# Performance work log

Measured on AMD Instinct MI355X. Metric: run time of the kernel, lower is better.

The kernel has to match this reference:

```python
import jax, jax.numpy as jnp
import numpy as np

M, D, G, E = 100000, 64, 1024, 1600000  # nodes, hidden, graphs, edges


def setup_inputs() -> dict:
    key = jax.random.key(0)
    k1, k2, k3, k4 = jax.random.split(key, 4)
    x = jax.random.normal(k1, (M, D), dtype=jnp.float32)
    batch = jnp.sort(jax.random.randint(k2, (M,), 0, G)).astype(jnp.int64)
    edge = jax.random.randint(k3, (2, E), 0, M).astype(jnp.int64)
    # nn.Linear(D, 1) parameters
    att_w = jax.random.normal(k4, (1, D), dtype=jnp.float32) * (1.0 / np.sqrt(D))
    att_b = jnp.zeros((1,), dtype=jnp.float32)
    return {"x": x, "att_w": att_w, "att_b": att_b, "batch": batch, "edge": edge}


def reference(x, att_w, att_b, batch, edge):
    # imp = attention(x): [M, 1] -> [M]
    imp = (x @ att_w.T + att_b)[:, 0]
    # scatter_softmax of imp over graph segments (batch)
    seg_max = jax.ops.segment_max(imp, batch, num_segments=G)
    e = jnp.exp(imp - seg_max[batch])
    denom = jax.ops.segment_sum(e, batch, num_segments=G)
    a = e / denom[batch]  # [M]
    # (degree branch is dead code when degree=False; degree softmax unused)
    # per-node weighted outer product imp_k * x_k x_k^T, scatter-summed per graph
    wj = (a[:, None] * x)[:, :, None] * x[:, None, :]  # [M, D, D]
    out = jax.ops.segment_sum(wj, batch, num_segments=G)  # [G, D, D]
    # Triuvec: upper-triangular (incl. diagonal) vectorization, row-major
    iu = jnp.triu_indices(D)
    return out[:, iu[0], iu[1]]  # [G, D*(D+1)/2]
```

## Files before the change

kernel.cpp:

```cpp
#include <hip/hip_runtime.h>
#include <math.h>


#define DDIM 64
#define NTRI 2080
#define CAP  2048
#define TILE 8

__device__ __forceinline__ float dot_row_w(const float* __restrict__ row,
                                           const float* __restrict__ sW) {
    float d = 0.f;
#pragma unroll
    for (int k = 0; k < 16; ++k) {
        const float4 v = ((const float4*)row)[k];
        const float4 w = ((const float4*)sW)[k];
        d = fmaf(v.x, w.x, d);
        d = fmaf(v.y, w.y, d);
        d = fmaf(v.z, w.z, d);
        d = fmaf(v.w, w.w, d);
    }
    return d;
}

__global__ void __launch_bounds__(256)
attention_sop_kernel(const float* __restrict__ x,
                     const float* __restrict__ att_w,
                     const float* __restrict__ att_b,
                     const int*   __restrict__ batch,
                     float*       __restrict__ out,
                     int M)
{
    const int g   = blockIdx.x;
    const int tid = threadIdx.x;

    __shared__ float sW[DDIM];
    __shared__ float sB;
    __shared__ float sImp[CAP];
    __shared__ float sRed[8];
    __shared__ float sXr[TILE * DDIM];
    __shared__ float sYs[TILE * DDIM];
    __shared__ int   sBounds[2];

    if (tid == 0) {
        int lo = 0, hi = M;
        while (lo < hi) { int mid = (lo + hi) >> 1; if (batch[mid] < g) lo = mid + 1; else hi = mid; }
        sBounds[0] = lo;
        int lo2 = lo, hi2 = M;
        while (lo2 < hi2) { int mid = (lo2 + hi2) >> 1; if (batch[mid] < g + 1) lo2 = mid + 1; else hi2 = mid; }
        sBounds[1] = lo2;
    }
    if (tid < DDIM) sW[tid] = att_w[tid];
    if (tid == DDIM) sB = att_b[0];
    __syncthreads();

    const int s = sBounds[0];
    const int e = sBounds[1];
    const int n = e - s;
    const float bb = sB;

    float* og = out + (size_t)g * NTRI;

    if (n == 0) {
        for (int idx = tid; idx < NTRI; idx += 256) og[idx] = 0.f;
        return;
    }

    float lmax = -INFINITY;
    for (int idx = tid; idx < n; idx += 256) {
        const float* row = x + (size_t)(s + idx) * DDIM;
        float d = dot_row_w(row, sW) + bb;
        if (idx < CAP) sImp[idx] = d;
        lmax = fmaxf(lmax, d);
    }
#pragma unroll
    for (int off = 32; off > 0; off >>= 1)
        lmax = fmaxf(lmax, __shfl_down(lmax, off, 64));
    const int wid = tid >> 6, lane = tid & 63;
    if (lane == 0) sRed[wid] = lmax;
    __syncthreads();
    if (tid == 0) {
        float mx = fmaxf(fmaxf(sRed[0], sRed[1]), fmaxf(sRed[2], sRed[3]));
        sRed[4] = mx;
    }
    __syncthreads();
    const float mx = sRed[4];

    float lsum = 0.f;
    for (int idx = tid; idx < n; idx += 256) {
        float d;
        if (idx < CAP) d = sImp[idx];
        else           d = dot_row_w(x + (size_t)(s + idx) * DDIM, sW) + bb;
        float ev = __expf(d - mx);
        if (idx < CAP) sImp[idx] = ev;
        lsum += ev;
    }
#pragma unroll
    for (int off = 32; off > 0; off >>= 1)
        lsum += __shfl_down(lsum, off, 64);
    if (lane == 0) sRed[wid] = lsum;
    __syncthreads();
    if (tid == 0) {
        float denom = sRed[0] + sRed[1] + sRed[2] + sRed[3];
        sRed[5] = 1.0f / denom;
    }
    __syncthreads();
    const float inv = sRed[5];

    const int ty = tid >> 4, tx = tid & 15;
    const int i0 = ty * 4, j0 = tx * 4;
    float acc[4][4];
#pragma unroll
    for (int a = 0; a < 4; ++a)
#pragma unroll
        for (int b = 0; b < 4; ++b) acc[a][b] = 0.f;

    for (int t0 = 0; t0 < n; t0 += TILE) {
        const int nt = min(TILE, n - t0);
        __syncthreads();
        for (int idx = tid; idx < nt * DDIM; idx += 256) {
            const int nn   = idx >> 6;
            const int gidx = t0 + nn;
            float c;
            if (gidx < CAP) {
                c = sImp[gidx] * inv;
            } else {
                float d  = dot_row_w(x + (size_t)(s + gidx) * DDIM, sW) + bb;
                c = __expf(d - mx) * inv;
            }
            const float v = x[(size_t)(s + t0) * DDIM + idx];
            sXr[idx] = v;
            sYs[idx] = v * c;
        }
        __syncthreads();
        for (int nn = 0; nn < nt; ++nn) {
            const float4 yi = *(const float4*)&sYs[nn * DDIM + i0];
            const float4 xj = *(const float4*)&sXr[nn * DDIM + j0];
            const float yv[4] = {yi.x, yi.y, yi.z, yi.w};
            const float xv[4] = {xj.x, xj.y, xj.z, xj.w};
#pragma unroll
            for (int a = 0; a < 4; ++a)
#pragma unroll
                for (int b = 0; b < 4; ++b)
                    acc[a][b] = fmaf(yv[a], xv[b], acc[a][b]);
        }
    }

#pragma unroll
    for (int a = 0; a < 4; ++a) {
        const int i = i0 + a;
        const int base = i * DDIM - (i * (i - 1)) / 2;
#pragma unroll
        for (int b = 0; b < 4; ++b) {
            const int j = j0 + b;
            if (j >= i) og[base + (j - i)] = acc[a][b];
        }
    }
}

extern "C" void kernel_launch(void* const* d_in, const int* in_sizes, int n_in,
                              void* d_out, int out_size, void* d_ws, size_t ws_size,
                              hipStream_t stream) {
    const float* x     = (const float*)d_in[0];
    const float* att_w = (const float*)d_in[1];
    const float* att_b = (const float*)d_in[2];
    const int*   batch = (const int*)d_in[3];
    float* out = (float*)d_out;

    const int M = in_sizes[0] / DDIM;
    const int G = out_size / NTRI;

    attention_sop_kernel<<<G, 256, 0, stream>>>(x, att_w, att_b, batch, out, M);
}
```

Baseline: 111.6 us.

## Split attention scores into a prep kernel and double-buffer node tiles in SOP kernel

Moves the per-node attention dot product and segment-boundary discovery into a separate fully parallel prep kernel that writes scores and segment starts to workspace. This replaces the per-block serial binary search and the repeated row dot products. The outer-product kernel now uses larger tiles of 32 nodes with register-prefetched double buffering, and applies the softmax weight on the fly instead of keeping a scaled copy. In exchange it adds a second launch and workspace traffic, and it relies on the workspace being large enough.

```diff
diff --git a/kernel.cpp b/kernel.cpp
--- a/kernel.cpp
+++ b/kernel.cpp
@@ -4,105 +4,96 @@
 
 #define DDIM 64
 #define NTRI 2080
-#define CAP  2048
-#define TILE 8
-
-__device__ __forceinline__ float dot_row_w(const float* __restrict__ row,
-                                           const float* __restrict__ sW) {
-    float d = 0.f;
-#pragma unroll
-    for (int k = 0; k < 16; ++k) {
-        const float4 v = ((const float4*)row)[k];
-        const float4 w = ((const float4*)sW)[k];
-        d = fmaf(v.x, w.x, d);
-        d = fmaf(v.y, w.y, d);
-        d = fmaf(v.z, w.z, d);
-        d = fmaf(v.w, w.w, d);
-    }
-    return d;
+#define CAP  1024
+#define TILE 32
+
+__global__ void __launch_bounds__(256)
+prep_kernel(const float* __restrict__ x,
+            const float* __restrict__ att_w,
+            const float* __restrict__ att_b,
+            const int*   __restrict__ batch,
+            float*       __restrict__ imp,
+            int*         __restrict__ seg_start,
+            int M, int G)
+{
+    const int tid    = threadIdx.x;
+    const int lane16 = tid & 15;
+    const int node   = blockIdx.x * 16 + (tid >> 4);
+
+    if (node < M) {
+        const float4 v = ((const float4*)x)[node * 16 + lane16];
+        const float4 w = ((const float4*)att_w)[lane16];
+        float d = fmaf(v.x, w.x, fmaf(v.y, w.y, fmaf(v.z, w.z, v.w * w.w)));
+        d += __shfl_down(d, 8, 16);
+        d += __shfl_down(d, 4, 16);
+        d += __shfl_down(d, 2, 16);
+        d += __shfl_down(d, 1, 16);
+        if (lane16 == 0) imp[node] = d + att_b[0];
+    }
+    if (tid < 16) {
+        const int m = blockIdx.x * 16 + tid;
+        if (m < M) {
+            const int b0 = batch[m];
+            if (m == 0) {
+                for (int g = 0; g <= b0; ++g) seg_start[g] = 0;
+            } else {
+                const int bp = batch[m - 1];
+                for (int g = bp + 1; g <= b0; ++g) seg_start[g] = m;
+            }
+            if (m == M - 1) {
+                for (int g = b0 + 1; g <= G; ++g) seg_start[g] = M;
+            }
+        }
+    }
 }
 
 __global__ void __launch_bounds__(256)
-attention_sop_kernel(const float* __restrict__ x,
-                     const float* __restrict__ att_w,
-                     const float* __restrict__ att_b,
-                     const int*   __restrict__ batch,
-                     float*       __restrict__ out,
-                     int M)
+sop_kernel(const float* __restrict__ x,
+           const float* __restrict__ imp,
+           const int*   __restrict__ seg_start,
+           float*       __restrict__ out,
+           int M)
 {
     const int g   = blockIdx.x;
     const int tid = threadIdx.x;
 
-    __shared__ float sW[DDIM];
-    __shared__ float sB;
-    __shared__ float sImp[CAP];
+    __shared__ float sA[CAP];
+    __shared__ float sX[2][TILE * DDIM];
+    __shared__ float sAt[2][TILE];
     __shared__ float sRed[8];
-    __shared__ float sXr[TILE * DDIM];
-    __shared__ float sYs[TILE * DDIM];
-    __shared__ int   sBounds[2];
-
-    if (tid == 0) {
-        int lo = 0, hi = M;
-        while (lo < hi) { int mid = (lo + hi) >> 1; if (batch[mid] < g) lo = mid + 1; else hi = mid; }
-        sBounds[0] = lo;
-        int lo2 = lo, hi2 = M;
-        while (lo2 < hi2) { int mid = (lo2 + hi2) >> 1; if (batch[mid] < g + 1) lo2 = mid + 1; else hi2 = mid; }
-        sBounds[1] = lo2;
-    }
-    if (tid < DDIM) sW[tid] = att_w[tid];
-    if (tid == DDIM) sB = att_b[0];
-    __syncthreads();
-
-    const int s = sBounds[0];
-    const int e = sBounds[1];
+
+    const int s = seg_start[g];
+    const int e = seg_start[g + 1];
     const int n = e - s;
-    const float bb = sB;
-
     float* og = out + (size_t)g * NTRI;
 
     if (n == 0) {
-        for (int idx = tid; idx < NTRI; idx += 256) og[idx] = 0.f;
+        for (int i = tid; i < NTRI; i += 256) og[i] = 0.f;
         return;
     }
 
     float lmax = -INFINITY;
-    for (int idx = tid; idx < n; idx += 256) {
-        const float* row = x + (size_t)(s + idx) * DDIM;
-        float d = dot_row_w(row, sW) + bb;
-        if (idx < CAP) sImp[idx] = d;
-        lmax = fmaxf(lmax, d);
-    }
-#pragma unroll
-    for (int off = 32; off > 0; off >>= 1)
-        lmax = fmaxf(lmax, __shfl_down(lmax, off, 64));
+    for (int i = tid; i < n; i += 256) lmax = fmaxf(lmax, imp[s + i]);
+#pragma unroll
+    for (int off = 32; off > 0; off >>= 1) lmax = fmaxf(lmax, __shfl_down(lmax, off, 64));
     const int wid = tid >> 6, lane = tid & 63;
     if (lane == 0) sRed[wid] = lmax;
     __syncthreads();
-    if (tid == 0) {
-        float mx = fmaxf(fmaxf(sRed[0], sRed[1]), fmaxf(sRed[2], sRed[3]));
-        sRed[4] = mx;
-    }
+    if (tid == 0) sRed[4] = fmaxf(fmaxf(sRed[0], sRed[1]), fmaxf(sRed[2], sRed[3]));
     __syncthreads();
     const float mx = sRed[4];
 
     float lsum = 0.f;
-    for (int idx = tid; idx < n; idx += 256) {
-        float d;
-        if (idx < CAP) d = sImp[idx];
-        else           d = dot_row_w(x + (size_t)(s + idx) * DDIM, sW) + bb;
-        float ev = __expf(d - mx);
-        if (idx < CAP) sImp[idx] = ev;
+    for (int i = tid; i < n; i += 256) {
+        const float ev = __expf(imp[s + i] - mx);
+        if (i < CAP) sA[i] = ev;
         lsum += ev;
     }
 #pragma unroll
-    for (int off = 32; off > 0; off >>= 1)
-        lsum += __shfl_down(lsum, off, 64);
+    for (int off = 32; off > 0; off >>= 1) lsum += __shfl_down(lsum, off, 64);
     if (lane == 0) sRed[wid] = lsum;
     __syncthreads();
-    if (tid == 0) {
-        float denom = sRed[0] + sRed[1] + sRed[2] + sRed[3];
-        sRed[5] = 1.0f / denom;
-    }
+    if (tid == 0) sRed[5] = 1.0f / (sRed[0] + sRed[1] + sRed[2] + sRed[3]);
     __syncthreads();
     const float inv = sRed[5];
 
@@ -114,34 +105,71 @@
 #pragma unroll
         for (int b = 0; b < 4; ++b) acc[a][b] = 0.f;
 
-    for (int t0 = 0; t0 < n; t0 += TILE) {
-        const int nt = min(TILE, n - t0);
+    const float4* x4 = (const float4*)x;
+    const int T = (n + TILE - 1) / TILE;
+
+    float4 r0, r1;
+    {
+        const int nt0 = min(TILE, n);
+        const long base = (long)s * 16;
+        const float4 z = {0.f, 0.f, 0.f, 0.f};
+        r0 = (tid       < nt0 * 16) ? x4[base + tid]       : z;
+        r1 = (tid + 256 < nt0 * 16) ? x4[base + tid + 256] : z;
+    }
+
+    for (int t = 0; t < T; ++t) {
+        const int t0  = t * TILE;
+        const int nt  = min(TILE, n - t0);
+        const int cur = t & 1;
+
+        ((float4*)sX[cur])[tid]       = r0;
+        ((float4*)sX[cur])[tid + 256] = r1;
+        if (tid < TILE) {
+            const int gidx = t0 + tid;
+            float av = 0.f;
+            if (gidx < n)
+                av = ((gidx < CAP) ? sA[gidx] : __expf(imp[s + gidx] - mx)) * inv;
+            sAt[cur][tid] = av;
+        }
+        if (t + 1 < T) {
+            const int t0n = t0 + TILE;
+            const int ntn = min(TILE, n - t0n);
+            const long base = (long)(s + t0n) * 16;
+            const float4 z = {0.f, 0.f, 0.f, 0.f};
+            r0 = (tid       < ntn * 16) ? x4[base + tid]       : z;
+            r1 = (tid + 256 < ntn * 16) ? x4[base + tid + 256] : z;
+        }
         __syncthreads();
-        for (int idx = tid; idx < nt * DDIM; idx += 256) {
-            const int nn   = idx >> 6;
-            const int gidx = t0 + nn;
-            float c;
-            if (gidx < CAP) {
-                c = sImp[gidx] * inv;
-            } else {
-                float d  = dot_row_w(x + (size_t)(s + gidx) * DDIM, sW) + bb;
-                c = __expf(d - mx) * inv;
-            }
-            const float v = x[(size_t)(s + t0) * DDIM + idx];
-            sXr[idx] = v;
-            sYs[idx] = v * c;
-        }
-        __syncthreads();
-        for (int nn = 0; nn < nt; ++nn) {
-            const float4 yi = *(const float4*)&sYs[nn * DDIM + i0];
-            const float4 xj = *(const float4*)&sXr[nn * DDIM + j0];
-            const float yv[4] = {yi.x, yi.y, yi.z, yi.w};
-            const float xv[4] = {xj.x, xj.y, xj.z, xj.w};
-#pragma unroll
-            for (int a = 0; a < 4; ++a)
-#pragma unroll
-                for (int b = 0; b < 4; ++b)
-                    acc[a][b] = fmaf(yv[a], xv[b], acc[a][b]);
+
+        const float* xb = sX[cur];
+        const float* ab = sAt[cur];
+        if (nt == TILE) {
+#pragma unroll 8
+            for (int nn = 0; nn < TILE; ++nn) {
+                const float c  = ab[nn];
+                const float4 xi = *(const float4*)&xb[nn * DDIM + i0];
+                const float4 xj = *(const float4*)&xb[nn * DDIM + j0];
+                const float yv[4] = {c * xi.x, c * xi.y, c * xi.z, c * xi.w};
+                const float xv[4] = {xj.x, xj.y, xj.z, xj.w};
+#pragma unroll
+                for (int a = 0; a < 4; ++a)
+#pragma unroll
+                    for (int b = 0; b < 4; ++b)
+                        acc[a][b] = fmaf(yv[a], xv[b], acc[a][b]);
+            }
+        } else {
+            for (int nn = 0; nn < nt; ++nn) {
+                const float c  = ab[nn];
+                const float4 xi = *(const float4*)&xb[nn * DDIM + i0];
+                const float4 xj = *(const float4*)&xb[nn * DDIM + j0];
+                const float yv[4] = {c * xi.x, c * xi.y, c * xi.z, c * xi.w};
+                const float xv[4] = {xj.x, xj.y, xj.z, xj.w};
+#pragma unroll
+                for (int a = 0; a < 4; ++a)
+#pragma unroll
+                    for (int b = 0; b < 4; ++b)
+                        acc[a][b] = fmaf(yv[a], xv[b], acc[a][b]);
+            }
         }
     }
 
@@ -169,5 +197,10 @@
     const int M = in_sizes[0] / DDIM;
     const int G = out_size / NTRI;
 
-    attention_sop_kernel<<<G, 256, 0, stream>>>(x, att_w, att_b, batch, out, M);
+    int*   seg_start = (int*)d_ws;
+    float* imp       = (float*)((char*)d_ws + 8192);
+
+    const int blocksA = (M + 15) / 16;
+    prep_kernel<<<blocksA, 256, 0, stream>>>(x, att_w, att_b, batch, imp, seg_start, M, G);
+    sop_kernel<<<G, 256, 0, stream>>>(x, imp, seg_start, out, M);
 }
```

After: 102.7 us. 8.0% less time.
